# Kernel tuning notes

Hardware: AMD Instinct MI355X
Metric: run time of the kernel (lower is better)

The kernel has to match this reference:

```python
import jax, jax.numpy as jnp
import numpy as np

NEG_SLOPE = 0.2

def setup_inputs() -> dict:
    key = jax.random.key(0)
    k1, k2, k3, k4, k5 = jax.random.split(key, 5)
    N_src, N_dst, E, H, D = 50000, 50000, 1600000, 8, 16
    return {
        "h_src": jax.random.normal(k1, (N_src, H * D), dtype=jnp.float32),
        "h_dst": jax.random.normal(k2, (N_dst, H * D), dtype=jnp.float32),
        "attn_l": jax.random.normal(k3, (1, H, D), dtype=jnp.float32),
        "src": jax.random.randint(k4, (E,), 0, N_src, dtype=jnp.int32),
        "dst": jax.random.randint(k5, (E,), 0, N_dst, dtype=jnp.int32),
    }

def reference(h_src, h_dst, attn_l, src, dst):
    N_dst = h_dst.shape[0]
    H, D = attn_l.shape[1], attn_l.shape[2]
    hs = h_src.reshape(-1, H, D)                       # [N_src, H, D]
    el = jnp.sum(hs * attn_l, axis=-1)                 # [N_src, H] per-node attn logit
    e = jax.nn.leaky_relu(el[src], NEG_SLOPE)          # [E, H] per-edge score
    # edge softmax over incoming edges of each dst node (stable)
    seg_max = jax.ops.segment_max(e, dst, num_segments=N_dst)   # [N_dst, H]
    ex = jnp.exp(e - seg_max[dst])                     # [E, H]
    denom = jax.ops.segment_sum(ex, dst, num_segments=N_dst)    # [N_dst, H]
    a = ex / denom[dst]                                # [E, H]
    # gather-multiply-scatter: u_mul_e then sum by dst
    m = hs[src] * a[:, :, None]                        # [E, H, D]
    out = jax.ops.segment_sum(m, dst, num_segments=N_dst)       # [N_dst, H, D]
    return out.reshape(N_dst, H * D)
```

## Files before the change

kernel.cpp:

```cpp
#include <hip/hip_runtime.h>

#define Hh 8
#define HD 128
#define NEG_SLOPE 0.2f
#define EPB 2048

__device__ __forceinline__ unsigned bfr(float f) {
    unsigned u = __float_as_uint(f);
    return (u + 0x7fffu + ((u >> 16) & 1u)) >> 16;
}
__device__ __forceinline__ unsigned pk(float a, float b) { return bfr(a) | (bfr(b) << 16); }

__global__ void k_b1(const int* __restrict__ dst, int* __restrict__ gh,
                     int E, int nblk, int nbkt,
                     const float* __restrict__ hs, const float* __restrict__ attn,
                     float* __restrict__ ew, uint4* __restrict__ hsb, int nh_src) {
    int t = threadIdx.x;
    if ((int)blockIdx.x < nblk) {
        __shared__ int lh[256];
        lh[t] = 0;
        __syncthreads();
        int i = blockIdx.x * EPB + t * 8;
        if (i + 7 < E) {
            int4 d0 = *(const int4*)(dst + i);
            int4 d1 = *(const int4*)(dst + i + 4);
            atomicAdd(&lh[d0.x >> 8], 1);
            atomicAdd(&lh[d0.y >> 8], 1);
            atomicAdd(&lh[d0.z >> 8], 1);
            atomicAdd(&lh[d0.w >> 8], 1);
            atomicAdd(&lh[d1.x >> 8], 1);
            atomicAdd(&lh[d1.y >> 8], 1);
            atomicAdd(&lh[d1.z >> 8], 1);
            atomicAdd(&lh[d1.w >> 8], 1);
        } else {
            for (int e = i; e < E; ++e) atomicAdd(&lh[dst[e] >> 8], 1);
        }
        __syncthreads();
        if (t < nbkt) gh[t * nblk + blockIdx.x] = lh[t];
    } else {
        int i = ((int)blockIdx.x - nblk) * 256 + t;
        if (i >= nh_src) return;
        int n = i >> 3, h = i & 7;
        const float4* a = (const float4*)(hs + (size_t)n * HD + h * 16);
        const float4* w = (const float4*)(attn + h * 16);
        float4 x0 = a[0], x1 = a[1], x2 = a[2], x3 = a[3];
        float4 w0 = w[0], w1 = w[1], w2 = w[2], w3 = w[3];
        float s = x0.x * w0.x + x0.y * w0.y + x0.z * w0.z + x0.w * w0.w
                + x1.x * w1.x + x1.y * w1.y + x1.z * w1.z + x1.w * w1.w
                + x2.x * w2.x + x2.y * w2.y + x2.z * w2.z + x2.w * w2.w
                + x3.x * w3.x + x3.y * w3.y + x3.z * w3.z + x3.w * w3.w;
        s = (s >= 0.f) ? s : NEG_SLOPE * s;
        ew[i] = __expf(s);
        uint4 p0 = { pk(x0.x, x0.y), pk(x0.z, x0.w), pk(x1.x, x1.y), pk(x1.z, x1.w) };
        uint4 p1 = { pk(x2.x, x2.y), pk(x2.z, x2.w), pk(x3.x, x3.y), pk(x3.z, x3.w) };
        hsb[(size_t)n * 16 + h * 2]     = p0;
        hsb[(size_t)n * 16 + h * 2 + 1] = p1;
    }
}

__global__ void k_gsum(const int* __restrict__ g, int* __restrict__ partial, int n) {
    __shared__ int sh[256];
    int t = threadIdx.x;
    int i = blockIdx.x * 256 + t;
    sh[t] = (i < n) ? g[i] : 0;
    __syncthreads();
    for (int off = 128; off > 0; off >>= 1) {
        if (t < off) sh[t] += sh[t + off];
        __syncthreads();
    }
    if (t == 0) partial[blockIdx.x] = sh[0];
}

__global__ void k_gscan1(int* __restrict__ partial, int nb) {
    __shared__ int sh[256];
    __shared__ int carry_s;
    int t = threadIdx.x;
    if (t == 0) carry_s = 0;
    __syncthreads();
    for (int base = 0; base < nb; base += 256) {
        int i = base + t;
        int v = (i < nb) ? partial[i] : 0;
        sh[t] = v;
        __syncthreads();
        for (int off = 1; off < 256; off <<= 1) {
            int x = (t >= off) ? sh[t - off] : 0;
            __syncthreads();
            sh[t] += x;
            __syncthreads();
        }
        int incl = sh[t];
        int carry = carry_s;
        if (i < nb) partial[i] = carry + incl - v;
        __syncthreads();
        if (t == 255) carry_s = carry + incl;
        __syncthreads();
    }
}

__global__ void k_gscan2(int* __restrict__ g, const int* __restrict__ partial, int n) {
    __shared__ int sh[256];
    int t = threadIdx.x;
    int i = blockIdx.x * 256 + t;
    int v = (i < n) ? g[i] : 0;
    sh[t] = v;
    __syncthreads();
    for (int off = 1; off < 256; off <<= 1) {
        int x = (t >= off) ? sh[t - off] : 0;
        __syncthreads();
        sh[t] += x;
        __syncthreads();
    }
    if (i < n) g[i] = partial[blockIdx.x] + sh[t] - v;
}

__global__ void k_b2(const int* __restrict__ src, const int* __restrict__ dst,
                     const int* __restrict__ gh, int* __restrict__ tmp,
                     int E, int nblk, int nbkt) {
    __shared__ int cur[256];
    int t = threadIdx.x, blk = blockIdx.x;
    if (t < nbkt) cur[t] = gh[t * nblk + blk];
    __syncthreads();
    int i = blk * EPB + t * 8;
    if (i + 7 < E) {
        int4 d0 = *(const int4*)(dst + i);
        int4 d1 = *(const int4*)(dst + i + 4);
        int4 s0 = *(const int4*)(src + i);
        int4 s1 = *(const int4*)(src + i + 4);
        int p;
        p = atomicAdd(&cur[d0.x >> 8], 1); tmp[p] = ((d0.x & 255) << 16) | s0.x;
        p = atomicAdd(&cur[d0.y >> 8], 1); tmp[p] = ((d0.y & 255) << 16) | s0.y;
        p = atomicAdd(&cur[d0.z >> 8], 1); tmp[p] = ((d0.z & 255) << 16) | s0.z;
        p = atomicAdd(&cur[d0.w >> 8], 1); tmp[p] = ((d0.w & 255) << 16) | s0.w;
        p = atomicAdd(&cur[d1.x >> 8], 1); tmp[p] = ((d1.x & 255) << 16) | s1.x;
        p = atomicAdd(&cur[d1.y >> 8], 1); tmp[p] = ((d1.y & 255) << 16) | s1.y;
        p = atomicAdd(&cur[d1.z >> 8], 1); tmp[p] = ((d1.z & 255) << 16) | s1.z;
        p = atomicAdd(&cur[d1.w >> 8], 1); tmp[p] = ((d1.w & 255) << 16) | s1.w;
    } else {
        for (int e = i; e < E; ++e) {
            int d = dst[e];
            int p = atomicAdd(&cur[d >> 8], 1);
            tmp[p] = ((d & 255) << 16) | src[e];
        }
    }
}

__global__ void __launch_bounds__(256)
k_b3(const int* __restrict__ gh, const int* __restrict__ tmp,
     int* __restrict__ adj, int* __restrict__ row_ptr,
     int E, int nblk, int nbkt, int ndst) {
    __shared__ int lh[256], sh[256], cur[256];
    int b = blockIdx.x, t = threadIdx.x;
    int s0 = gh[b * nblk];
    int s1 = (b + 1 < nbkt) ? gh[(b + 1) * nblk] : E;
    lh[t] = 0;
    __syncthreads();
    for (int j = s0 + t; j < s1; j += 256)
        atomicAdd(&lh[tmp[j] >> 16], 1);
    __syncthreads();
    int v = lh[t];
    sh[t] = v;
    __syncthreads();
    for (int off = 1; off < 256; off <<= 1) {
        int x = (t >= off) ? sh[t - off] : 0;
        __syncthreads();
        sh[t] += x;
        __syncthreads();
    }
    int start = s0 + sh[t] - v;
    cur[t] = start;
    int d = b * 256 + t;
    if (d < ndst) row_ptr[d] = start;
    if (b == nbkt - 1 && t == 0) row_ptr[ndst] = E;
    __syncthreads();
    for (int j = s0 + t; j < s1; j += 256) {
        int w = tmp[j];
        int pos = atomicAdd(&cur[w >> 16], 1);
        adj[pos] = w & 0xffff;
    }
}

__global__ void __launch_bounds__(128)
k_agg(const int* __restrict__ row_ptr, const int* __restrict__ adj,
      const uint4* __restrict__ hsb, const float* __restrict__ ew,
      float* __restrict__ out) {
    int d = blockIdx.x;
    int t = threadIdx.x;
    int j0 = row_ptr[d], j1 = row_ptr[d + 1];
    int q = t & 15;
    int slot = t >> 4;
    int h = q >> 1;

    float4 a0 = {0.f, 0.f, 0.f, 0.f}, a1 = {0.f, 0.f, 0.f, 0.f};
    float ws = 0.f;
    int j = j0 + slot;
    for (; j + 8 < j1; j += 16) {
        int s0 = adj[j], s1 = adj[j + 8];
        float w0 = ew[s0 * Hh + h], w1 = ew[s1 * Hh + h];
        uint4 x0 = hsb[(size_t)s0 * 16 + q];
        uint4 x1 = hsb[(size_t)s1 * 16 + q];
        a0.x += __uint_as_float(x0.x << 16) * w0;
        a0.y += __uint_as_float(x0.x & 0xffff0000u) * w0;
        a0.z += __uint_as_float(x0.y << 16) * w0;
        a0.w += __uint_as_float(x0.y & 0xffff0000u) * w0;
        a1.x += __uint_as_float(x0.z << 16) * w0;
        a1.y += __uint_as_float(x0.z & 0xffff0000u) * w0;
        a1.z += __uint_as_float(x0.w << 16) * w0;
        a1.w += __uint_as_float(x0.w & 0xffff0000u) * w0;
        a0.x += __uint_as_float(x1.x << 16) * w1;
        a0.y += __uint_as_float(x1.x & 0xffff0000u) * w1;
        a0.z += __uint_as_float(x1.y << 16) * w1;
        a0.w += __uint_as_float(x1.y & 0xffff0000u) * w1;
        a1.x += __uint_as_float(x1.z << 16) * w1;
        a1.y += __uint_as_float(x1.z & 0xffff0000u) * w1;
        a1.z += __uint_as_float(x1.w << 16) * w1;
        a1.w += __uint_as_float(x1.w & 0xffff0000u) * w1;
        ws += w0 + w1;
    }
    if (j < j1) {
        int s0 = adj[j];
        float w0 = ew[s0 * Hh + h];
        uint4 x0 = hsb[(size_t)s0 * 16 + q];
        a0.x += __uint_as_float(x0.x << 16) * w0;
        a0.y += __uint_as_float(x0.x & 0xffff0000u) * w0;
        a0.z += __uint_as_float(x0.y << 16) * w0;
        a0.w += __uint_as_float(x0.y & 0xffff0000u) * w0;
        a1.x += __uint_as_float(x0.z << 16) * w0;
        a1.y += __uint_as_float(x0.z & 0xffff0000u) * w0;
        a1.z += __uint_as_float(x0.w << 16) * w0;
        a1.w += __uint_as_float(x0.w & 0xffff0000u) * w0;
        ws += w0;
    }

#pragma unroll
    for (int off = 16; off <= 32; off <<= 1) {
        a0.x += __shfl_xor(a0.x, off, 64);
        a0.y += __shfl_xor(a0.y, off, 64);
        a0.z += __shfl_xor(a0.z, off, 64);
        a0.w += __shfl_xor(a0.w, off, 64);
        a1.x += __shfl_xor(a1.x, off, 64);
        a1.y += __shfl_xor(a1.y, off, 64);
        a1.z += __shfl_xor(a1.z, off, 64);
        a1.w += __shfl_xor(a1.w, off, 64);
        ws   += __shfl_xor(ws,   off, 64);
    }
    __shared__ float4 sp0[16], sp1[16];
    __shared__ float wsp[16];
    if (t >= 64 && t < 80) { sp0[q] = a0; sp1[q] = a1; wsp[q] = ws; }
    __syncthreads();
    if (t < 16) {
        float wt = ws + wsp[t];
        float r = (wt > 0.f) ? 1.0f / wt : 0.f;
        float4 o0 = sp0[t], o1 = sp1[t];
        o0.x = (a0.x + o0.x) * r; o0.y = (a0.y + o0.y) * r;
        o0.z = (a0.z + o0.z) * r; o0.w = (a0.w + o0.w) * r;
        o1.x = (a1.x + o1.x) * r; o1.y = (a1.y + o1.y) * r;
        o1.z = (a1.z + o1.z) * r; o1.w = (a1.w + o1.w) * r;
        float4* op = (float4*)(out + (size_t)d * HD + t * 8);
        op[0] = o0;
        op[1] = o1;
    }
}

extern "C" void kernel_launch(void* const* d_in, const int* in_sizes, int n_in,
                              void* d_out, int out_size, void* d_ws, size_t ws_size,
                              hipStream_t stream) {
    const float* h_src  = (const float*)d_in[0];
    const float* attn_l = (const float*)d_in[2];
    const int*   src    = (const int*)d_in[3];
    const int*   dst    = (const int*)d_in[4];
    float* out = (float*)d_out;

    const int N_src = in_sizes[0] / HD;
    const int N_dst = in_sizes[1] / HD;
    const int E     = in_sizes[3];
    const int NH_src = N_src * Hh;

    const int NBLK = (E + EPB - 1) / EPB;
    const int NBKT = (N_dst + 255) / 256;
    const int M    = NBKT * NBLK;
    const int NC   = (M + 255) / 256;
    const int NB_EW = (NH_src + 255) / 256;

    unsigned short* hsb = (unsigned short*)d_ws;
    float* ew      = (float*)(hsb + (size_t)N_src * HD);
    int*   tmp     = (int*)(ew + NH_src);
    int*   adj     = tmp + E;
    int*   gh      = adj + E;
    int*   partial = gh + M;
    int*   row_ptr = partial + NC;

    k_b1<<<NBLK + NB_EW, 256, 0, stream>>>(dst, gh, E, NBLK, NBKT,
                                           h_src, attn_l, ew, (uint4*)hsb, NH_src);
    k_gsum  <<<NC, 256, 0, stream>>>(gh, partial, M);
    k_gscan1<<<1, 256, 0, stream>>>(partial, NC);
    k_gscan2<<<NC, 256, 0, stream>>>(gh, partial, M);
    k_b2<<<NBLK, 256, 0, stream>>>(src, dst, gh, tmp, E, NBLK, NBKT);
    k_b3<<<NBKT, 256, 0, stream>>>(gh, tmp, adj, row_ptr, E, NBLK, NBKT, N_dst);
    k_agg<<<N_dst, 128, 0, stream>>>(row_ptr, adj, (const uint4*)hsb, ew, out);
}
```

Baseline: 208.2 us.

## Fuse scan kernels, double edges per block, 16-bit adjacency, unroll aggregation by four

Merges the single-block partial scan into the per-block scan kernel: each block recomputes its prefix by summing all earlier partials, which removes one launch and its serial dependency. Doubles edges per block in the histogram and scatter passes, halving the number of histogram columns to scan. Stores adjacency as 16-bit indices to halve its memory traffic, and unrolls the aggregation loop to four gathers in flight per thread for more memory-level parallelism. The risks are redundant prefix summation across blocks, higher register pressure in the aggregation kernel, and the 16-bit index format, which only works while N_src fits in 16 bits.

```diff
diff --git a/kernel.cpp b/kernel.cpp
--- a/kernel.cpp
+++ b/kernel.cpp
@@ -3,7 +3,8 @@
 #define Hh 8
 #define HD 128
 #define NEG_SLOPE 0.2f
-#define EPB 2048
+#define EPB 4096
+
 
 __device__ __forceinline__ unsigned bfr(float f) {
     unsigned u = __float_as_uint(f);
@@ -20,18 +21,16 @@
         __shared__ int lh[256];
         lh[t] = 0;
         __syncthreads();
-        int i = blockIdx.x * EPB + t * 8;
-        if (i + 7 < E) {
-            int4 d0 = *(const int4*)(dst + i);
-            int4 d1 = *(const int4*)(dst + i + 4);
-            atomicAdd(&lh[d0.x >> 8], 1);
-            atomicAdd(&lh[d0.y >> 8], 1);
-            atomicAdd(&lh[d0.z >> 8], 1);
-            atomicAdd(&lh[d0.w >> 8], 1);
-            atomicAdd(&lh[d1.x >> 8], 1);
-            atomicAdd(&lh[d1.y >> 8], 1);
-            atomicAdd(&lh[d1.z >> 8], 1);
-            atomicAdd(&lh[d1.w >> 8], 1);
+        int i = blockIdx.x * EPB + t * 16;
+        if (i + 15 < E) {
+#pragma unroll
+            for (int k = 0; k < 16; k += 4) {
+                int4 d = *(const int4*)(dst + i + k);
+                atomicAdd(&lh[d.x >> 8], 1);
+                atomicAdd(&lh[d.y >> 8], 1);
+                atomicAdd(&lh[d.z >> 8], 1);
+                atomicAdd(&lh[d.w >> 8], 1);
+            }
         } else {
             for (int e = i; e < E; ++e) atomicAdd(&lh[dst[e] >> 8], 1);
         }
@@ -71,37 +70,24 @@
     if (t == 0) partial[blockIdx.x] = sh[0];
 }
 
-__global__ void k_gscan1(int* __restrict__ partial, int nb) {
+__global__ void k_gscan(int* __restrict__ g, const int* __restrict__ partial, int n) {
     __shared__ int sh[256];
-    __shared__ int carry_s;
-    int t = threadIdx.x;
-    if (t == 0) carry_s = 0;
-    __syncthreads();
-    for (int base = 0; base < nb; base += 256) {
-        int i = base + t;
-        int v = (i < nb) ? partial[i] : 0;
-        sh[t] = v;
-        __syncthreads();
-        for (int off = 1; off < 256; off <<= 1) {
-            int x = (t >= off) ? sh[t - off] : 0;
-            __syncthreads();
-            sh[t] += x;
-            __syncthreads();
-        }
-        int incl = sh[t];
-        int carry = carry_s;
-        if (i < nb) partial[i] = carry + incl - v;
-        __syncthreads();
-        if (t == 255) carry_s = carry + incl;
-        __syncthreads();
-    }
-}
-
-__global__ void k_gscan2(int* __restrict__ g, const int* __restrict__ partial, int n) {
-    __shared__ int sh[256];
-    int t = threadIdx.x;
+    __shared__ int pre_s;
+    int t = threadIdx.x;
+    int acc = 0;
+    for (int k = t; k < (int)blockIdx.x; k += 256) acc += partial[k];
+    sh[t] = acc;
+    __syncthreads();
+    for (int off = 128; off > 0; off >>= 1) {
+        if (t < off) sh[t] += sh[t + off];
+        __syncthreads();
+    }
+    if (t == 0) pre_s = sh[0];
+    __syncthreads();
+    int pre = pre_s;
     int i = blockIdx.x * 256 + t;
     int v = (i < n) ? g[i] : 0;
+    __syncthreads();
     sh[t] = v;
     __syncthreads();
     for (int off = 1; off < 256; off <<= 1) {
@@ -110,7 +96,7 @@
         sh[t] += x;
         __syncthreads();
     }
-    if (i < n) g[i] = partial[blockIdx.x] + sh[t] - v;
+    if (i < n) g[i] = pre + sh[t] - v;
 }
 
 __global__ void k_b2(const int* __restrict__ src, const int* __restrict__ dst,
@@ -120,21 +106,18 @@
     int t = threadIdx.x, blk = blockIdx.x;
     if (t < nbkt) cur[t] = gh[t * nblk + blk];
     __syncthreads();
-    int i = blk * EPB + t * 8;
-    if (i + 7 < E) {
-        int4 d0 = *(const int4*)(dst + i);
-        int4 d1 = *(const int4*)(dst + i + 4);
-        int4 s0 = *(const int4*)(src + i);
-        int4 s1 = *(const int4*)(src + i + 4);
-        int p;
-        p = atomicAdd(&cur[d0.x >> 8], 1); tmp[p] = ((d0.x & 255) << 16) | s0.x;
-        p = atomicAdd(&cur[d0.y >> 8], 1); tmp[p] = ((d0.y & 255) << 16) | s0.y;
-        p = atomicAdd(&cur[d0.z >> 8], 1); tmp[p] = ((d0.z & 255) << 16) | s0.z;
-        p = atomicAdd(&cur[d0.w >> 8], 1); tmp[p] = ((d0.w & 255) << 16) | s0.w;
-        p = atomicAdd(&cur[d1.x >> 8], 1); tmp[p] = ((d1.x & 255) << 16) | s1.x;
-        p = atomicAdd(&cur[d1.y >> 8], 1); tmp[p] = ((d1.y & 255) << 16) | s1.y;
-        p = atomicAdd(&cur[d1.z >> 8], 1); tmp[p] = ((d1.z & 255) << 16) | s1.z;
-        p = atomicAdd(&cur[d1.w >> 8], 1); tmp[p] = ((d1.w & 255) << 16) | s1.w;
+    int i = blk * EPB + t * 16;
+    if (i + 15 < E) {
+#pragma unroll
+        for (int k = 0; k < 16; k += 4) {
+            int4 d = *(const int4*)(dst + i + k);
+            int4 s = *(const int4*)(src + i + k);
+            int p;
+            p = atomicAdd(&cur[d.x >> 8], 1); tmp[p] = ((d.x & 255) << 16) | s.x;
+            p = atomicAdd(&cur[d.y >> 8], 1); tmp[p] = ((d.y & 255) << 16) | s.y;
+            p = atomicAdd(&cur[d.z >> 8], 1); tmp[p] = ((d.z & 255) << 16) | s.z;
+            p = atomicAdd(&cur[d.w >> 8], 1); tmp[p] = ((d.w & 255) << 16) | s.w;
+        }
     } else {
         for (int e = i; e < E; ++e) {
             int d = dst[e];
@@ -146,7 +129,7 @@
 
 __global__ void __launch_bounds__(256)
 k_b3(const int* __restrict__ gh, const int* __restrict__ tmp,
-     int* __restrict__ adj, int* __restrict__ row_ptr,
+     unsigned short* __restrict__ adj, int* __restrict__ row_ptr,
      int E, int nblk, int nbkt, int ndst) {
     __shared__ int lh[256], sh[256], cur[256];
     int b = blockIdx.x, t = threadIdx.x;
@@ -175,12 +158,22 @@
     for (int j = s0 + t; j < s1; j += 256) {
         int w = tmp[j];
         int pos = atomicAdd(&cur[w >> 16], 1);
-        adj[pos] = w & 0xffff;
-    }
-}
+        adj[pos] = (unsigned short)(w & 0xffff);
+    }
+}
+
+#define ACC8(X, W) \
+    a0.x += __uint_as_float((X).x << 16) * (W); \
+    a0.y += __uint_as_float((X).x & 0xffff0000u) * (W); \
+    a0.z += __uint_as_float((X).y << 16) * (W); \
+    a0.w += __uint_as_float((X).y & 0xffff0000u) * (W); \
+    a1.x += __uint_as_float((X).z << 16) * (W); \
+    a1.y += __uint_as_float((X).z & 0xffff0000u) * (W); \
+    a1.z += __uint_as_float((X).w << 16) * (W); \
+    a1.w += __uint_as_float((X).w & 0xffff0000u) * (W);
 
 __global__ void __launch_bounds__(128)
-k_agg(const int* __restrict__ row_ptr, const int* __restrict__ adj,
+k_agg(const int* __restrict__ row_ptr, const unsigned short* __restrict__ adj,
       const uint4* __restrict__ hsb, const float* __restrict__ ew,
       float* __restrict__ out) {
     int d = blockIdx.x;
@@ -193,41 +186,25 @@
     float4 a0 = {0.f, 0.f, 0.f, 0.f}, a1 = {0.f, 0.f, 0.f, 0.f};
     float ws = 0.f;
     int j = j0 + slot;
-    for (; j + 8 < j1; j += 16) {
-        int s0 = adj[j], s1 = adj[j + 8];
+    for (; j + 24 < j1; j += 32) {
+        int s0 = adj[j], s1 = adj[j + 8], s2 = adj[j + 16], s3 = adj[j + 24];
         float w0 = ew[s0 * Hh + h], w1 = ew[s1 * Hh + h];
+        float w2 = ew[s2 * Hh + h], w3 = ew[s3 * Hh + h];
         uint4 x0 = hsb[(size_t)s0 * 16 + q];
         uint4 x1 = hsb[(size_t)s1 * 16 + q];
-        a0.x += __uint_as_float(x0.x << 16) * w0;
-        a0.y += __uint_as_float(x0.x & 0xffff0000u) * w0;
-        a0.z += __uint_as_float(x0.y << 16) * w0;
-        a0.w += __uint_as_float(x0.y & 0xffff0000u) * w0;
-        a1.x += __uint_as_float(x0.z << 16) * w0;
-        a1.y += __uint_as_float(x0.z & 0xffff0000u) * w0;
-        a1.z += __uint_as_float(x0.w << 16) * w0;
-        a1.w += __uint_as_float(x0.w & 0xffff0000u) * w0;
-        a0.x += __uint_as_float(x1.x << 16) * w1;
-        a0.y += __uint_as_float(x1.x & 0xffff0000u) * w1;
-        a0.z += __uint_as_float(x1.y << 16) * w1;
-        a0.w += __uint_as_float(x1.y & 0xffff0000u) * w1;
-        a1.x += __uint_as_float(x1.z << 16) * w1;
-        a1.y += __uint_as_float(x1.z & 0xffff0000u) * w1;
-        a1.z += __uint_as_float(x1.w << 16) * w1;
-        a1.w += __uint_as_float(x1.w & 0xffff0000u) * w1;
-        ws += w0 + w1;
-    }
-    if (j < j1) {
+        uint4 x2 = hsb[(size_t)s2 * 16 + q];
+        uint4 x3 = hsb[(size_t)s3 * 16 + q];
+        ACC8(x0, w0)
+        ACC8(x1, w1)
+        ACC8(x2, w2)
+        ACC8(x3, w3)
+        ws += w0 + w1 + w2 + w3;
+    }
+    for (; j < j1; j += 8) {
         int s0 = adj[j];
         float w0 = ew[s0 * Hh + h];
         uint4 x0 = hsb[(size_t)s0 * 16 + q];
-        a0.x += __uint_as_float(x0.x << 16) * w0;
-        a0.y += __uint_as_float(x0.x & 0xffff0000u) * w0;
-        a0.z += __uint_as_float(x0.y << 16) * w0;
-        a0.w += __uint_as_float(x0.y & 0xffff0000u) * w0;
-        a1.x += __uint_as_float(x0.z << 16) * w0;
-        a1.y += __uint_as_float(x0.z & 0xffff0000u) * w0;
-        a1.z += __uint_as_float(x0.w << 16) * w0;
-        a1.w += __uint_as_float(x0.w & 0xffff0000u) * w0;
+        ACC8(x0, w0)
         ws += w0;
     }
 
@@ -284,16 +261,15 @@
     unsigned short* hsb = (unsigned short*)d_ws;
     float* ew      = (float*)(hsb + (size_t)N_src * HD);
     int*   tmp     = (int*)(ew + NH_src);
-    int*   adj     = tmp + E;
-    int*   gh      = adj + E;
+    unsigned short* adj = (unsigned short*)(tmp + E);
+    int*   gh      = (int*)(adj + (((size_t)E + 1) & ~(size_t)1));
     int*   partial = gh + M;
     int*   row_ptr = partial + NC;
 
     k_b1<<<NBLK + NB_EW, 256, 0, stream>>>(dst, gh, E, NBLK, NBKT,
                                            h_src, attn_l, ew, (uint4*)hsb, NH_src);
-    k_gsum  <<<NC, 256, 0, stream>>>(gh, partial, M);
-    k_gscan1<<<1, 256, 0, stream>>>(partial, NC);
-    k_gscan2<<<NC, 256, 0, stream>>>(gh, partial, M);
+    k_gsum <<<NC, 256, 0, stream>>>(gh, partial, M);
+    k_gscan<<<NC, 256, 0, stream>>>(gh, partial, M);
     k_b2<<<NBLK, 256, 0, stream>>>(src, dst, gh, tmp, E, NBLK, NBKT);
     k_b3<<<NBKT, 256, 0, stream>>>(gh, tmp, adj, row_ptr, E, NBLK, NBKT, N_dst);
     k_agg<<<N_dst, 128, 0, stream>>>(row_ptr, adj, (const uint4*)hsb, ew, out);
```

After: 201.2 us. 3.4% less time.
